# Kernel optimization log

Hardware: AMD Instinct MI355X
Metric: run time of the kernel (lower is better)

The kernel has to match this reference:

```python
import jax, jax.numpy as jnp
import numpy as np

HIDDEN = 4096
N_HEADS = 32
QK_NOPE = 128
QK_ROPE = 64
QK_HEAD = QK_NOPE + QK_ROPE  # 192
V_HEAD = 128
Q_LORA = 1536
KV_LORA = 512
EPS = 1e-6
ROPE_BASE = 10000.0
T = 2048


def rmsnorm(x, g, eps=EPS):
    var = jnp.mean(x * x, axis=-1, keepdims=True)
    return x * jax.lax.rsqrt(var + eps) * g


def apply_rope_interleaved(x, cos, sin):
    # non-neox style: rotate interleaved pairs. x: [T, ..., d]; cos/sin: [T, d//2]
    x1 = x[..., 0::2]
    x2 = x[..., 1::2]
    while cos.ndim < x1.ndim:
        cos = cos[:, None]
        sin = sin[:, None]
    o1 = x1 * cos - x2 * sin
    o2 = x1 * sin + x2 * cos
    return jnp.stack([o1, o2], axis=-1).reshape(x.shape)


def setup_inputs() -> dict:
    key = jax.random.key(0)
    ks = jax.random.split(key, 8)
    s = lambda fan_in: 1.0 / np.sqrt(fan_in)
    return {
        "positions": jnp.arange(T, dtype=jnp.int32),
        "hidden_states": jax.random.normal(ks[0], (T, HIDDEN), jnp.float32),
        "wq_a": jax.random.normal(ks[1], (HIDDEN, Q_LORA), jnp.float32) * s(HIDDEN),
        "gq": jnp.ones((Q_LORA,), jnp.float32),
        "wq_b": jax.random.normal(ks[2], (Q_LORA, N_HEADS * QK_HEAD), jnp.float32) * s(Q_LORA),
        "wkv_a": jax.random.normal(ks[3], (HIDDEN, KV_LORA + QK_ROPE), jnp.float32) * s(HIDDEN),
        "gkv": jnp.ones((KV_LORA,), jnp.float32),
        "wkv_b": jax.random.normal(ks[4], (KV_LORA, N_HEADS * (QK_NOPE + V_HEAD)), jnp.float32) * s(KV_LORA),
        "wo": jax.random.normal(ks[5], (N_HEADS * V_HEAD, HIDDEN), jnp.float32) * s(N_HEADS * V_HEAD),
    }


def reference(positions, hidden_states, wq_a, gq, wq_b, wkv_a, gkv, wkv_b, wo):
    t = hidden_states.shape[0]
    scale = QK_HEAD ** -0.5

    # Q path: low-rank down-proj -> RMSNorm -> up-proj
    q = rmsnorm(hidden_states @ wq_a, gq) @ wq_b  # [T, H*192]
    q = q.reshape(t, N_HEADS, QK_HEAD)
    q_nope, q_pe = q[..., :QK_NOPE], q[..., QK_NOPE:]

    # KV path: compressed latent + decoupled rope key
    kv_a = hidden_states @ wkv_a  # [T, kv_lora + rope]
    c_kv, k_pe = kv_a[:, :KV_LORA], kv_a[:, KV_LORA:]
    kv = rmsnorm(c_kv, gkv) @ wkv_b  # [T, H*(nope+v)]
    kv = kv.reshape(t, N_HEADS, QK_NOPE + V_HEAD)
    k_nope, v = kv[..., :QK_NOPE], kv[..., QK_NOPE:]

    # RoPE (interleaved / non-neox)
    inv_freq = 1.0 / (ROPE_BASE ** (jnp.arange(0, QK_ROPE, 2, dtype=jnp.float32) / QK_ROPE))
    angles = positions.astype(jnp.float32)[:, None] * inv_freq[None, :]  # [T, rope/2]
    cos, sin = jnp.cos(angles), jnp.sin(angles)
    q_pe = apply_rope_interleaved(q_pe, cos, sin)          # [T, H, rope]
    k_pe = apply_rope_interleaved(k_pe, cos, sin)          # [T, rope]

    q_full = jnp.concatenate([q_nope, q_pe], axis=-1)       # [T, H, 192]
    k_full = jnp.concatenate(
        [k_nope, jnp.broadcast_to(k_pe[:, None, :], (t, N_HEADS, QK_ROPE))], axis=-1)

    scores = jnp.einsum('qhd,khd->hqk', q_full, k_full) * scale  # [H, T, T]
    causal = positions[:, None] >= positions[None, :]
    scores = jnp.where(causal[None], scores, jnp.finfo(scores.dtype).min)
    probs = jax.nn.softmax(scores, axis=-1)
    attn = jnp.einsum('hqk,khd->qhd', probs, v)              # [T, H, 128]
    return attn.reshape(t, N_HEADS * V_HEAD) @ wo            # [T, hidden]
```

## Files before the change

kernel.cpp:

```cpp
#include <hip/hip_runtime.h>
#include <hip/hip_bf16.h>
#include <stdint.h>

typedef __hip_bfloat16 bf16;
typedef unsigned short u16;
typedef short v8s __attribute__((ext_vector_type(8)));
typedef float v4f __attribute__((ext_vector_type(4)));

#define T_LEN   2048
#define HIDDEN  4096
#define N_HEADS 32
#define QK_NOPE 128
#define QK_ROPE 64
#define QK_HEAD 192
#define V_HEAD  128
#define Q_LORA  1536
#define KV_LORA 512
#define NFUSE   2176

enum { DT_BF16 = 0, DT_F32 = 1, DT_EXT = 2 };

__device__ __forceinline__ u16 f2b(float x) {
    union { bf16 h; u16 u; } cv; cv.h = __float2bfloat16(x); return cv.u;
}

typedef const __attribute__((address_space(1))) uint32_t* gas_ptr;
typedef __attribute__((address_space(3))) uint32_t* las_ptr;
__device__ __forceinline__ void gll16(const void* g, void* l) {
    __builtin_amdgcn_global_load_lds((gas_ptr)g, (las_ptr)l, 16, 0, 0);
}

__global__ __launch_bounds__(256) void convert_bf16(
    const void* __restrict__ X, u16* __restrict__ Y, int nelem,
    const uint32_t* __restrict__ probe)
{
    const bool f32 = (probe[0] & 0xFFFFu) == 0u;
    const int i = (blockIdx.x * 256 + threadIdx.x) * 8;
    if (i >= nelem) return;
    if (f32) {
        const float* x = (const float*)X + i;
        u16 o[8];
        #pragma unroll
        for (int e = 0; e < 8; ++e) o[e] = f2b(x[e]);
        *(uint4*)(Y + i) = *(const uint4*)o;
    } else {
        *(uint4*)(Y + i) = *(const uint4*)((const u16*)X + i);
    }
}

__global__ __launch_bounds__(256) void transpose_to_bf16(
    const void* __restrict__ W, u16* __restrict__ Wt,
    int K, int N, const uint32_t* __restrict__ probe)
{
    const bool f32 = (probe[0] & 0xFFFFu) == 0u;
    __shared__ uint32_t Ts[64 * 33];
    const int n0 = blockIdx.x * 64;
    const int k0 = blockIdx.y * 64;
    const int tid = threadIdx.x;
    {
        const int nc = (tid & 7) * 8;
        const int kp = tid >> 3;
        const int k = k0 + kp * 2;
        uint32_t vals[8];
        if (n0 >= N) {
            #pragma unroll
            for (int e = 0; e < 8; ++e) vals[e] = 0;
        } else if (f32) {
            const float* w0 = (const float*)W + (size_t)k * N + n0 + nc;
            const float* w1 = w0 + N;
            #pragma unroll
            for (int e = 0; e < 8; ++e)
                vals[e] = (uint32_t)f2b(w0[e]) | ((uint32_t)f2b(w1[e]) << 16);
        } else {
            const u16* w0 = (const u16*)W + (size_t)k * N + n0 + nc;
            const u16* w1 = w0 + N;
            u16 a[8], b[8];
            *(uint4*)a = *(const uint4*)w0;
            *(uint4*)b = *(const uint4*)w1;
            #pragma unroll
            for (int e = 0; e < 8; ++e)
                vals[e] = (uint32_t)a[e] | ((uint32_t)b[e] << 16);
        }
        #pragma unroll
        for (int e = 0; e < 8; ++e)
            Ts[(nc + e) * 33 + kp] = vals[e];
    }
    __syncthreads();
    {
        const int n = tid >> 2;
        const int kp0 = (tid & 3) * 8;
        u16 out[16];
        #pragma unroll
        for (int j = 0; j < 8; ++j) {
            const uint32_t v = Ts[n * 33 + kp0 + j];
            out[2 * j]     = (u16)(v & 0xFFFFu);
            out[2 * j + 1] = (u16)(v >> 16);
        }
        u16* dst = Wt + (size_t)(n0 + n) * K + k0 + kp0 * 2;
        *(uint4*)dst = *(const uint4*)out;
        *(uint4*)(dst + 8) = *(const uint4*)(out + 8);
    }
}

__global__ __launch_bounds__(256) void gemm_bt(
    const u16* __restrict__ A, const u16* __restrict__ Bt,
    void* __restrict__ C, int ccode,
    int N, int K, const uint32_t* __restrict__ probe)
{
    __shared__ __align__(16) u16 As[128 * 32];
    __shared__ __align__(16) u16 Bs[128 * 32];

    const int tid  = threadIdx.x;
    const int lane = tid & 63;
    const int wave = tid >> 6;
    const int quad = lane >> 4, l15 = lane & 15;
    const int wr = (wave >> 1) * 64, wc = (wave & 1) * 64;

    const int gx  = gridDim.x;
    const int nwg = gx * gridDim.y;
    int bid = blockIdx.y * gx + blockIdx.x;
    if ((nwg & 7) == 0)
        bid = (bid & 7) * (nwg >> 3) + (bid >> 3);
    const int bxl = bid % gx;
    const int byl = bid / gx;
    const size_t brow = (size_t)byl * 128;
    const size_t bcol = (size_t)bxl * 128;

    v4f acc[4][4];
    #pragma unroll
    for (int i = 0; i < 4; ++i)
        #pragma unroll
        for (int j = 0; j < 4; ++j)
            acc[i][j] = (v4f){0.f, 0.f, 0.f, 0.f};

    const int c0 = tid, c1 = tid + 256;
    const int r0 = c0 >> 2, e0 = (c0 & 3) * 8;
    const int r1 = c1 >> 2, e1 = (c1 & 3) * 8;
    const u16* Ab = A + brow * K;
    const u16* Bb = Bt + bcol * K;

    for (int k0 = 0; k0 < K; k0 += 32) {
        gll16(Ab + (size_t)r0 * K + k0 + e0, (void*)(As + c0 * 8));
        gll16(Ab + (size_t)r1 * K + k0 + e1, (void*)(As + c1 * 8));
        gll16(Bb + (size_t)r0 * K + k0 + e0, (void*)(Bs + c0 * 8));
        gll16(Bb + (size_t)r1 * K + k0 + e1, (void*)(Bs + c1 * 8));
        __syncthreads();

        v8s af[4], bf[4];
        #pragma unroll
        for (int i = 0; i < 4; ++i)
            af[i] = *(const v8s*)(As + (wr + i * 16 + l15) * 32 + quad * 8);
        #pragma unroll
        for (int j = 0; j < 4; ++j)
            bf[j] = *(const v8s*)(Bs + (wc + j * 16 + l15) * 32 + quad * 8);
        #pragma unroll
        for (int i = 0; i < 4; ++i)
            #pragma unroll
            for (int j = 0; j < 4; ++j)
                acc[i][j] = __builtin_amdgcn_mfma_f32_16x16x32_bf16(
                    af[i], bf[j], acc[i][j], 0, 0, 0);
        __syncthreads();
    }

    const bool c_f32 = (ccode == DT_F32) ||
                       (ccode == DT_EXT && (probe[0] & 0xFFFFu) == 0u);
    #pragma unroll
    for (int i = 0; i < 4; ++i) {
        #pragma unroll
        for (int r = 0; r < 4; ++r) {
            const size_t row = brow + wr + i * 16 + quad * 4 + r;
            #pragma unroll
            for (int j = 0; j < 4; ++j) {
                const size_t col = bcol + wc + j * 16 + l15;
                if (c_f32) ((float*)C)[row * N + col] = acc[i][j][r];
                else       ((u16*)C)[row * N + col]   = f2b(acc[i][j][r]);
            }
        }
    }
}

__global__ __launch_bounds__(256) void rmsnorm_kernel(
    const float* __restrict__ x, const void* __restrict__ g,
    bf16* __restrict__ y, int cols,
    const uint32_t* __restrict__ probe)
{
    const bool g_f32 = (probe[0] & 0xFFFFu) == 0u;
    const int row = blockIdx.x;
    const float* xr = x + (size_t)row * NFUSE;
    float ss = 0.f;
    for (int c = threadIdx.x; c < cols; c += 256) {
        float v = xr[c];
        ss += v * v;
    }
    #pragma unroll
    for (int off = 32; off > 0; off >>= 1) ss += __shfl_down(ss, off, 64);
    __shared__ float wsum[4];
    const int wave = threadIdx.x >> 6, lane = threadIdx.x & 63;
    if (lane == 0) wsum[wave] = ss;
    __syncthreads();
    const float tot = wsum[0] + wsum[1] + wsum[2] + wsum[3];
    const float inv = rsqrtf(tot / (float)cols + 1e-6f);
    for (int c = threadIdx.x; c < cols; c += 256) {
        const float gv = g_f32 ? ((const float*)g)[c]
                               : __bfloat162float(((const bf16*)g)[c]);
        y[(size_t)row * cols + c] = __float2bfloat16(xr[c] * inv * gv);
    }
}

__global__ void kpe_rope_kernel(const float* __restrict__ qkv,
                                const int* __restrict__ pos,
                                bf16* __restrict__ kpe)
{
    const int t = blockIdx.x;
    const int i = threadIdx.x;
    const float x1 = qkv[(size_t)t * NFUSE + 2048 + 2 * i];
    const float x2 = qkv[(size_t)t * NFUSE + 2048 + 2 * i + 1];
    const float inv_freq = powf(10000.f, -(float)(2 * i) / 64.f);
    const float ang = (float)pos[t] * inv_freq;
    float s, c;
    sincosf(ang, &s, &c);
    kpe[(size_t)t * 64 + 2 * i]     = __float2bfloat16(x1 * c - x2 * s);
    kpe[(size_t)t * 64 + 2 * i + 1] = __float2bfloat16(x1 * s + x2 * c);
}

__global__ __launch_bounds__(256) void qpe_rope_kernel(bf16* __restrict__ q,
                                                       const int* __restrict__ pos)
{
    const int idx = blockIdx.x * 256 + threadIdx.x;
    const int i = idx & 31;
    const int h = (idx >> 5) & 31;
    const int t = idx >> 10;
    if (t >= T_LEN) return;
    bf16* base = q + ((size_t)t * N_HEADS + h) * QK_HEAD + QK_NOPE + 2 * i;
    const float x1 = __bfloat162float(base[0]);
    const float x2 = __bfloat162float(base[1]);
    const float inv_freq = powf(10000.f, -(float)(2 * i) / 64.f);
    const float ang = (float)pos[t] * inv_freq;
    float s, c;
    sincosf(ang, &s, &c);
    base[0] = __float2bfloat16(x1 * c - x2 * s);
    base[1] = __float2bfloat16(x1 * s + x2 * c);
}

#define KS_LD 200
#define VT_LD 72
#define PS_LD 72

__global__ __launch_bounds__(256) void attn_mfma(
    const bf16* __restrict__ qg, const bf16* __restrict__ kvg,
    const bf16* __restrict__ kpeg, bf16* __restrict__ attng)
{
    __shared__ u16 Ks[64 * KS_LD];
    __shared__ u16 Vt[V_HEAD * VT_LD];
    __shared__ u16 Ps[4 * 32 * PS_LD];

    const int bx = blockIdx.x;
    const int h  = bx & 31;
    const int qt = 15 - (bx >> 5);
    const int q0 = qt * 128;
    const int nkt = 2 * qt + 2;

    const int tid  = threadIdx.x;
    const int wave = tid >> 6, lane = tid & 63;
    const int quad = lane >> 4, l15 = lane & 15;
    const float scale = 0.07216878364870323f;

    v8s qf[2][6];
    #pragma unroll
    for (int mi = 0; mi < 2; ++mi)
        #pragma unroll
        for (int ks = 0; ks < 6; ++ks)
            qf[mi][ks] = *(const v8s*)((const u16*)qg +
                (size_t)(q0 + wave * 32 + mi * 16 + l15) * 6144 +
                h * 192 + ks * 32 + quad * 8);

    v4f accO[2][8];
    #pragma unroll
    for (int mi = 0; mi < 2; ++mi)
        #pragma unroll
        for (int vs = 0; vs < 8; ++vs)
            accO[mi][vs] = (v4f){0.f, 0.f, 0.f, 0.f};
    float m_run[2][4], l_run[2][4];
    #pragma unroll
    for (int mi = 0; mi < 2; ++mi)
        #pragma unroll
        for (int r = 0; r < 4; ++r) { m_run[mi][r] = -1e30f; l_run[mi][r] = 0.f; }

    for (int kt = 0; kt < nkt; ++kt) {
        const int k0 = kt * 64;
        __syncthreads();
        {
            const int jj = tid >> 4;
            const int c0 = (tid & 15) * 16;
            #pragma unroll
            for (int p = 0; p < 4; ++p) {
                const int j = jj + p * 16;
                const u16* src = (const u16*)kvg +
                    (size_t)(k0 + j) * 8192 + h * 256 + c0;
                uint4 v0 = *(const uint4*)src;
                uint4 v1 = *(const uint4*)(src + 8);
                if (c0 < 128) {
                    u16* dst = &Ks[j * KS_LD + c0];
                    *(uint4*)dst = v0;
                    *(uint4*)(dst + 8) = v1;
                } else {
                    u16 buf[16];
                    *(uint4*)buf = v0;
                    *(uint4*)(buf + 8) = v1;
                    const int d0 = c0 - 128;
                    #pragma unroll
                    for (int e = 0; e < 16; ++e) {
                        const int d = d0 + e;
                        const int jswz = j ^ (((d >> 4) & 7) << 3);
                        Vt[d * VT_LD + jswz] = buf[e];
                    }
                }
            }
            const int j2 = tid >> 2;
            const int c2 = (tid & 3) * 16;
            const u16* src = (const u16*)kpeg + (size_t)(k0 + j2) * 64 + c2;
            uint4 w0 = *(const uint4*)src;
            uint4 w1 = *(const uint4*)(src + 8);
            u16* dst = &Ks[j2 * KS_LD + 128 + c2];
            *(uint4*)dst = w0;
            *(uint4*)(dst + 8) = w1;
        }
        __syncthreads();

        v4f accS[2][4];
        #pragma unroll
        for (int mi = 0; mi < 2; ++mi)
            #pragma unroll
            for (int nj = 0; nj < 4; ++nj)
                accS[mi][nj] = (v4f){0.f, 0.f, 0.f, 0.f};
        #pragma unroll
        for (int ks = 0; ks < 6; ++ks) {
            v8s kf[4];
            #pragma unroll
            for (int nj = 0; nj < 4; ++nj)
                kf[nj] = *(const v8s*)&Ks[(nj * 16 + l15) * KS_LD + ks * 32 + quad * 8];
            #pragma unroll
            for (int mi = 0; mi < 2; ++mi)
                #pragma unroll
                for (int nj = 0; nj < 4; ++nj)
                    accS[mi][nj] = __builtin_amdgcn_mfma_f32_16x16x32_bf16(
                        qf[mi][ks], kf[nj], accS[mi][nj], 0, 0, 0);
        }

        const bool need_mask = (kt >= 2 * qt);
        float p[2][4][4];
        float alpha[2][4];
        #pragma unroll
        for (int mi = 0; mi < 2; ++mi) {
            #pragma unroll
            for (int r = 0; r < 4; ++r) {
                const int qrow = q0 + wave * 32 + mi * 16 + quad * 4 + r;
                float sv[4];
                float rm = -1e30f;
                #pragma unroll
                for (int nj = 0; nj < 4; ++nj) {
                    float s = accS[mi][nj][r] * scale;
                    if (need_mask) {
                        const int jgl = k0 + nj * 16 + l15;
                        if (jgl > qrow) s = -1e30f;
                    }
                    sv[nj] = s;
                    rm = fmaxf(rm, s);
                }
                rm = fmaxf(rm, __shfl_xor(rm, 1));
                rm = fmaxf(rm, __shfl_xor(rm, 2));
                rm = fmaxf(rm, __shfl_xor(rm, 4));
                rm = fmaxf(rm, __shfl_xor(rm, 8));
                const float mo = m_run[mi][r];
                const float mn = fmaxf(mo, rm);
                const float al = __expf(mo - mn);
                float ps = 0.f;
                #pragma unroll
                for (int nj = 0; nj < 4; ++nj) {
                    const float pv = __expf(sv[nj] - mn);
                    p[mi][nj][r] = pv;
                    ps += pv;
                }
                ps += __shfl_xor(ps, 1);
                ps += __shfl_xor(ps, 2);
                ps += __shfl_xor(ps, 4);
                ps += __shfl_xor(ps, 8);
                l_run[mi][r] = l_run[mi][r] * al + ps;
                m_run[mi][r] = mn;
                alpha[mi][r] = al;
            }
        }

        #pragma unroll
        for (int mi = 0; mi < 2; ++mi)
            #pragma unroll
            for (int vs = 0; vs < 8; ++vs)
                #pragma unroll
                for (int r = 0; r < 4; ++r)
                    accO[mi][vs][r] *= alpha[mi][r];

        u16* psw = &Ps[wave * 32 * PS_LD];
        #pragma unroll
        for (int mi = 0; mi < 2; ++mi)
            #pragma unroll
            for (int nj = 0; nj < 4; ++nj)
                #pragma unroll
                for (int r = 0; r < 4; ++r)
                    psw[(mi * 16 + quad * 4 + r) * PS_LD + nj * 16 + l15] =
                        f2b(p[mi][nj][r]);

        #pragma unroll
        for (int kf = 0; kf < 2; ++kf) {
            v8s pf[2];
            #pragma unroll
            for (int mi = 0; mi < 2; ++mi)
                pf[mi] = *(const v8s*)&psw[(mi * 16 + l15) * PS_LD + kf * 32 + quad * 8];
            #pragma unroll
            for (int vs = 0; vs < 8; ++vs) {
                const int swz = (vs & 7) << 3;
                v8s vf = *(const v8s*)&Vt[(vs * 16 + l15) * VT_LD +
                                          ((kf * 32 + quad * 8) ^ swz)];
                #pragma unroll
                for (int mi = 0; mi < 2; ++mi)
                    accO[mi][vs] = __builtin_amdgcn_mfma_f32_16x16x32_bf16(
                        pf[mi], vf, accO[mi][vs], 0, 0, 0);
            }
        }
    }

    #pragma unroll
    for (int mi = 0; mi < 2; ++mi) {
        #pragma unroll
        for (int r = 0; r < 4; ++r) {
            const int qrow = q0 + wave * 32 + mi * 16 + quad * 4 + r;
            const float linv = 1.f / l_run[mi][r];
            #pragma unroll
            for (int vs = 0; vs < 8; ++vs)
                attng[(size_t)qrow * 4096 + h * 128 + vs * 16 + l15] =
                    __float2bfloat16(accO[mi][vs][r] * linv);
        }
    }
}

extern "C" void kernel_launch(void* const* d_in, const int* in_sizes, int n_in,
                              void* d_out, int out_size, void* d_ws, size_t ws_size,
                              hipStream_t stream)
{
    const int*  pos    = (const int*)d_in[0];
    const void* hidden = d_in[1];
    const void* wq_a   = d_in[2];
    const void* gq     = d_in[3];
    const void* wq_b   = d_in[4];
    const void* wkv_a  = d_in[5];
    const void* gkv    = d_in[6];
    const void* wkv_b  = d_in[7];
    const void* wo     = d_in[8];
    const uint32_t* probe = (const uint32_t*)gq;

    char* w = (char*)d_ws;
    u16*   h_bf   = (u16*)w;   w += (size_t)T_LEN * HIDDEN * 2;
    u16*   Wt_qkv = (u16*)w;   w += (size_t)NFUSE * HIDDEN * 2;
    u16*   Wt_qb  = (u16*)w;   w += (size_t)6144 * Q_LORA * 2;
    u16*   Wt_kvb = (u16*)w;   w += (size_t)8192 * KV_LORA * 2;
    u16*   Wt_o   = (u16*)w;   w += (size_t)HIDDEN * HIDDEN * 2;
    float* qkv    = (float*)w; w += (size_t)T_LEN * NFUSE * 4;
    u16*   q_norm = (u16*)w;   w += (size_t)T_LEN * Q_LORA * 2;
    u16*   q      = (u16*)w;   w += (size_t)T_LEN * N_HEADS * QK_HEAD * 2;
    u16*   ckv    = (u16*)w;   w += (size_t)T_LEN * KV_LORA * 2;
    u16*   kpe    = (u16*)w;   w += (size_t)T_LEN * QK_ROPE * 2;
    u16*   kv     = (u16*)w;   w += (size_t)T_LEN * N_HEADS * 256 * 2;
    u16*   attn   = Wt_qkv;

    convert_bf16<<<4096, 256, 0, stream>>>(hidden, h_bf, T_LEN * HIDDEN, probe);
    transpose_to_bf16<<<dim3(1536 / 64, HIDDEN / 64), 256, 0, stream>>>(
        wq_a, Wt_qkv, HIDDEN, 1536, probe);
    transpose_to_bf16<<<dim3(640 / 64, HIDDEN / 64), 256, 0, stream>>>(
        wkv_a, Wt_qkv + (size_t)1536 * HIDDEN, HIDDEN, 576, probe);
    transpose_to_bf16<<<dim3(6144 / 64, Q_LORA / 64), 256, 0, stream>>>(
        wq_b, Wt_qb, Q_LORA, 6144, probe);
    transpose_to_bf16<<<dim3(8192 / 64, KV_LORA / 64), 256, 0, stream>>>(
        wkv_b, Wt_kvb, KV_LORA, 8192, probe);
    transpose_to_bf16<<<dim3(HIDDEN / 64, HIDDEN / 64), 256, 0, stream>>>(
        wo, Wt_o, HIDDEN, HIDDEN, probe);

    gemm_bt<<<dim3(NFUSE / 128, T_LEN / 128), 256, 0, stream>>>(
        h_bf, Wt_qkv, qkv, DT_F32, NFUSE, HIDDEN, probe);

    rmsnorm_kernel<<<T_LEN, 256, 0, stream>>>(qkv, gq, (bf16*)q_norm, Q_LORA, probe);
    rmsnorm_kernel<<<T_LEN, 256, 0, stream>>>(qkv + 1536, gkv, (bf16*)ckv, KV_LORA, probe);
    kpe_rope_kernel<<<T_LEN, 32, 0, stream>>>(qkv, pos, (bf16*)kpe);

    gemm_bt<<<dim3(6144 / 128, T_LEN / 128), 256, 0, stream>>>(
        q_norm, Wt_qb, q, DT_BF16, 6144, Q_LORA, probe);
    qpe_rope_kernel<<<(T_LEN * N_HEADS * 32) / 256, 256, 0, stream>>>((bf16*)q, pos);

    gemm_bt<<<dim3(8192 / 128, T_LEN / 128), 256, 0, stream>>>(
        ckv, Wt_kvb, kv, DT_BF16, 8192, KV_LORA, probe);

    attn_mfma<<<dim3(N_HEADS * (T_LEN / 128)), 256, 0, stream>>>(
        (const bf16*)q, (const bf16*)kv, (const bf16*)kpe, (bf16*)attn);

    gemm_bt<<<dim3(HIDDEN / 128, T_LEN / 128), 256, 0, stream>>>(
        attn, Wt_o, d_out, DT_EXT, HIDDEN, HIDDEN, probe);
}
```

Measured before the change: 754.4 us.

## Shrink attention P staging buffer and register footprint to fit three blocks per CU

The per-wave P staging buffer is halved, so the P·V product now stages one 32-key half at a time. The softmax probabilities are stored back into the score accumulator registers instead of separate p/alpha arrays, and the accumulator rescale is folded into the per-row loop. A minimum of three resident blocks is requested through launch bounds. The aim is to cut LDS and VGPR use so more attention blocks can be resident and latency is better hidden. The cost is more interleaved LDS write/read steps and a 72-byte row stride that is not 16-byte aligned for the 128-bit P reads, which may be slower or split.

Result: slower. 1.308 ms (+73.4%).

```diff
diff --git a/kernel.cpp b/kernel.cpp
--- a/kernel.cpp
+++ b/kernel.cpp
@@ -244,9 +244,9 @@
 
 #define KS_LD 200
 #define VT_LD 72
-#define PS_LD 72
-
-__global__ __launch_bounds__(256) void attn_mfma(
+#define PS_LD 36
+
+__global__ __launch_bounds__(256, 3) void attn_mfma(
     const bf16* __restrict__ qg, const bf16* __restrict__ kvg,
     const bf16* __restrict__ kpeg, bf16* __restrict__ attng)
 {
@@ -348,14 +348,11 @@
         }
 
         const bool need_mask = (kt >= 2 * qt);
-        float p[2][4][4];
-        float alpha[2][4];
         #pragma unroll
         for (int mi = 0; mi < 2; ++mi) {
             #pragma unroll
             for (int r = 0; r < 4; ++r) {
                 const int qrow = q0 + wave * 32 + mi * 16 + quad * 4 + r;
-                float sv[4];
                 float rm = -1e30f;
                 #pragma unroll
                 for (int nj = 0; nj < 4; ++nj) {
@@ -364,7 +361,7 @@
                         const int jgl = k0 + nj * 16 + l15;
                         if (jgl > qrow) s = -1e30f;
                     }
-                    sv[nj] = s;
+                    accS[mi][nj][r] = s;
                     rm = fmaxf(rm, s);
                 }
                 rm = fmaxf(rm, __shfl_xor(rm, 1));
@@ -374,11 +371,12 @@
                 const float mo = m_run[mi][r];
                 const float mn = fmaxf(mo, rm);
                 const float al = __expf(mo - mn);
+                m_run[mi][r] = mn;
                 float ps = 0.f;
                 #pragma unroll
                 for (int nj = 0; nj < 4; ++nj) {
-                    const float pv = __expf(sv[nj] - mn);
-                    p[mi][nj][r] = pv;
+                    const float pv = __expf(accS[mi][nj][r] - mn);
+                    accS[mi][nj][r] = pv;
                     ps += pv;
                 }
                 ps += __shfl_xor(ps, 1);
@@ -386,40 +384,32 @@
                 ps += __shfl_xor(ps, 4);
                 ps += __shfl_xor(ps, 8);
                 l_run[mi][r] = l_run[mi][r] * al + ps;
-                m_run[mi][r] = mn;
-                alpha[mi][r] = al;
+                #pragma unroll
+                for (int vs = 0; vs < 8; ++vs)
+                    accO[mi][vs][r] *= al;
             }
         }
 
-        #pragma unroll
-        for (int mi = 0; mi < 2; ++mi)
-            #pragma unroll
-            for (int vs = 0; vs < 8; ++vs)
-                #pragma unroll
-                for (int r = 0; r < 4; ++r)
-                    accO[mi][vs][r] *= alpha[mi][r];
-
         u16* psw = &Ps[wave * 32 * PS_LD];
         #pragma unroll
-        for (int mi = 0; mi < 2; ++mi)
-            #pragma unroll
-            for (int nj = 0; nj < 4; ++nj)
-                #pragma unroll
-                for (int r = 0; r < 4; ++r)
-                    psw[(mi * 16 + quad * 4 + r) * PS_LD + nj * 16 + l15] =
-                        f2b(p[mi][nj][r]);
-
-        #pragma unroll
-        for (int kf = 0; kf < 2; ++kf) {
+        for (int kf2 = 0; kf2 < 2; ++kf2) {
+            #pragma unroll
+            for (int mi = 0; mi < 2; ++mi)
+                #pragma unroll
+                for (int njh = 0; njh < 2; ++njh)
+                    #pragma unroll
+                    for (int r = 0; r < 4; ++r)
+                        psw[(mi * 16 + quad * 4 + r) * PS_LD + njh * 16 + l15] =
+                            f2b(accS[mi][kf2 * 2 + njh][r]);
             v8s pf[2];
             #pragma unroll
             for (int mi = 0; mi < 2; ++mi)
-                pf[mi] = *(const v8s*)&psw[(mi * 16 + l15) * PS_LD + kf * 32 + quad * 8];
+                pf[mi] = *(const v8s*)&psw[(mi * 16 + l15) * PS_LD + quad * 8];
             #pragma unroll
             for (int vs = 0; vs < 8; ++vs) {
                 const int swz = (vs & 7) << 3;
                 v8s vf = *(const v8s*)&Vt[(vs * 16 + l15) * VT_LD +
-                                          ((kf * 32 + quad * 8) ^ swz)];
+                                          ((kf2 * 32 + quad * 8) ^ swz)];
                 #pragma unroll
                 for (int mi = 0; mi < 2; ++mi)
                     accO[mi][vs] = __builtin_amdgcn_mfma_f32_16x16x32_bf16(
```
